# Performance work log

Measured on AMD Instinct MI355X. Metric: run time of the kernel, lower is better.

The kernel has to match this reference:

```python
import jax, jax.numpy as jnp
import numpy as np

N_NODES = 50000
N_EDGES = 800000
NUM_GRAPHS = 4
IN_DIM, HID_DIM, OUT_DIM = 1024, 128, 1
MAX_RISK = 5.0


def gcn_conv(x, W, b, src, dst, n):
    """PyG GCNConv: add self-loops, sym-normalize, gather-GEMM-scatter."""
    loop = jnp.arange(n, dtype=src.dtype)
    s = jnp.concatenate([src, loop])
    d = jnp.concatenate([dst, loop])
    deg = jax.ops.segment_sum(jnp.ones_like(d, dtype=x.dtype), d, num_segments=n)
    dinv = jnp.where(deg > 0, jax.lax.rsqrt(deg), 0.0)
    norm = dinv[s] * dinv[d]  # [E+N]
    xw = x @ W                # dense GEMM first (fewer FLOPs than per-edge)
    msg = xw[s] * norm[:, None]          # irregular gather, [E+N, out]
    out = jax.ops.segment_sum(msg, d, num_segments=n)  # scatter-add
    return out + b


def setup_inputs() -> dict:
    key = jax.random.key(0)
    ks = jax.random.split(key, 12)
    x = jax.random.normal(ks[0], (N_NODES, IN_DIM), dtype=jnp.float32)
    edge_index = jax.random.randint(ks[1], (2, N_EDGES), 0, N_NODES, dtype=jnp.int64)
    batch = jnp.sort(jax.random.randint(ks[2], (N_NODES,), 0, NUM_GRAPHS, dtype=jnp.int64))

    def glorot(k, fan_in, fan_out):
        s = np.sqrt(6.0 / (fan_in + fan_out)).astype(np.float32)
        return jax.random.uniform(k, (fan_in, fan_out), jnp.float32, -s, s)

    params = {
        'W0': glorot(ks[3], IN_DIM, HID_DIM),  'b0': jnp.zeros((HID_DIM,), jnp.float32),
        'W1': glorot(ks[4], HID_DIM, HID_DIM), 'b1': jnp.zeros((HID_DIM,), jnp.float32),
        'W2': glorot(ks[5], HID_DIM, HID_DIM), 'b2': jnp.zeros((HID_DIM,), jnp.float32),
        'Wl1': glorot(ks[6], 2 * HID_DIM, HID_DIM), 'bl1': jnp.zeros((HID_DIM,), jnp.float32),
        'Wl2': glorot(ks[7], HID_DIM, HID_DIM // 2), 'bl2': jnp.zeros((HID_DIM // 2,), jnp.float32),
        'Wl3': glorot(ks[8], HID_DIM // 2, OUT_DIM), 'bl3': jnp.zeros((OUT_DIM,), jnp.float32),
    }
    return dict(x=x, edge_index=edge_index, batch=batch, **params)


def reference(x, edge_index, batch, W0, b0, W1, b1, W2, b2, Wl1, bl1, Wl2, bl2, Wl3, bl3):
    n = x.shape[0]
    src, dst = edge_index[0], edge_index[1]
    h = jax.nn.relu(gcn_conv(x, W0, b0, src, dst, n))
    h = jax.nn.relu(gcn_conv(h, W1, b1, src, dst, n))
    h = jax.nn.relu(gcn_conv(h, W2, b2, src, dst, n))
    # global max pool + global mean pool per graph
    gmax = jax.ops.segment_max(h, batch, num_segments=NUM_GRAPHS)
    gsum = jax.ops.segment_sum(h, batch, num_segments=NUM_GRAPHS)
    cnt = jax.ops.segment_sum(jnp.ones((n,), h.dtype), batch, num_segments=NUM_GRAPHS)
    gmean = gsum / jnp.maximum(cnt, 1.0)[:, None]
    g = jnp.concatenate([gmax, gmean], axis=1)  # [G, 2*hid]
    g = jax.nn.relu(g @ Wl1 + bl1)
    g = jax.nn.relu(g @ Wl2 + bl2)
    out = g @ Wl3 + bl3
    return jnp.minimum(out, MAX_RISK)
```

## Files before the change

kernel.cpp:

```cpp
#include <hip/hip_runtime.h>
#include <math.h>

#define HID 128
#define NGRAPH 4

typedef int idx_t;
typedef float f32x4 __attribute__((ext_vector_type(4)));
typedef _Float16 h8 __attribute__((ext_vector_type(8)));

__global__ __launch_bounds__(256) void k_count(const idx_t* __restrict__ dst,
                                               int* __restrict__ cnt, int E) {
  int e = blockIdx.x * 256 + threadIdx.x;
  if (e < E) atomicAdd(&cnt[dst[e]], 1);
}

#define SC 1024
__global__ __launch_bounds__(256) void k_scan1(const int* __restrict__ cnt,
                                               int* __restrict__ bsum, int n) {
  __shared__ int sh[256];
  int base = blockIdx.x * SC + threadIdx.x * 4;
  int s = 0;
#pragma unroll
  for (int j = 0; j < 4; ++j) { int i = base + j; if (i < n) s += cnt[i]; }
  sh[threadIdx.x] = s;
  __syncthreads();
  for (int o = 128; o > 0; o >>= 1) {
    if (threadIdx.x < o) sh[threadIdx.x] += sh[threadIdx.x + o];
    __syncthreads();
  }
  if (threadIdx.x == 0) bsum[blockIdx.x] = sh[0];
}

__global__ __launch_bounds__(64) void k_scan2(const int* __restrict__ bsum,
                                              int* __restrict__ boff,
                                              int* __restrict__ off, int nb, int n) {
  int lane = threadIdx.x;
  int v = (lane < nb) ? bsum[lane] : 0;
  for (int d = 1; d < 64; d <<= 1) {
    int t = __shfl_up(v, d);
    if (lane >= d) v += t;
  }
  int ex = __shfl_up(v, 1);
  if (lane == 0) ex = 0;
  if (lane < nb) boff[lane] = ex;
  if (lane == nb - 1) off[n] = v;
}

__global__ __launch_bounds__(256) void k_scan3(const int* __restrict__ cnt,
                                               const int* __restrict__ boff,
                                               int* __restrict__ off,
                                               float* __restrict__ dinv, int n) {
  __shared__ int sh[256];
  int base = blockIdx.x * SC + threadIdx.x * 4;
  int c[4];
  int s = 0;
#pragma unroll
  for (int j = 0; j < 4; ++j) {
    int i = base + j;
    c[j] = (i < n) ? cnt[i] : 0;
    s += c[j];
  }
  sh[threadIdx.x] = s;
  __syncthreads();
  for (int o = 1; o < 256; o <<= 1) {
    int t = (threadIdx.x >= (unsigned)o) ? sh[threadIdx.x - o] : 0;
    __syncthreads();
    sh[threadIdx.x] += t;
    __syncthreads();
  }
  int ex = sh[threadIdx.x] - s + boff[blockIdx.x];
#pragma unroll
  for (int j = 0; j < 4; ++j) {
    int i = base + j;
    if (i < n) {
      off[i] = ex;
      dinv[i] = 1.0f / sqrtf((float)c[j] + 1.0f);
      ex += c[j];
    }
  }
}

__global__ __launch_bounds__(256) void k_fill(const idx_t* __restrict__ src,
                                              const idx_t* __restrict__ dst,
                                              const int* __restrict__ off,
                                              const float* __restrict__ dinv,
                                              int* __restrict__ fillc,
                                              int2* __restrict__ edata, int E) {
  int e = blockIdx.x * 256 + threadIdx.x;
  if (e < E) {
    int s = src[e], d = dst[e];
    int p = atomicAdd(&fillc[d], 1);
    float w = dinv[s] * dinv[d];
    edata[off[d] + p] = make_int2(s, __float_as_int(w));
  }
}

__global__ __launch_bounds__(256) void k_wsplitf(const float* __restrict__ W,
                                                 _Float16* __restrict__ Wh,
                                                 _Float16* __restrict__ Wl, int K) {
  int i = blockIdx.x * 256 + threadIdx.x;
  if (i >= K * HID) return;
  int j = i & 7, lane = (i >> 3) & 63, ni = (i >> 9) & 7, t = i >> 12;
  int k = t * 32 + (lane >> 4) * 8 + j;
  int col = ni * 16 + (lane & 15);
  float f = W[(size_t)k * HID + col];
  _Float16 h = (_Float16)f;
  Wh[i] = h;
  Wl[i] = (_Float16)(f - (float)h);
}

template <int K, bool F32>
__global__ __launch_bounds__(256, 4) void k_gemm5(const void* __restrict__ Xv,
                                                  const _Float16* __restrict__ Wfh,
                                                  const _Float16* __restrict__ Wfl,
                                                  _Float16* __restrict__ Y16, int M) {
  constexpr int KPW = K / 4;
  constexpr int NT = KPW / 32;
  const int tid = threadIdx.x;
  const int wid = tid >> 6, lane = tid & 63;
  const int lrow = lane & 15, kg = lane >> 4;
  const int row0 = blockIdx.x * 32;
  const int ra = row0 + lrow, rb = row0 + 16 + lrow;
  const int rca = (ra < M) ? ra : 0, rcb = (rb < M) ? rb : 0;
  const float* xf0 = (const float*)Xv + (size_t)rca * K + wid * KPW + kg * 8;
  const float* xf1 = (const float*)Xv + (size_t)rcb * K + wid * KPW + kg * 8;
  const _Float16* xg0 = (const _Float16*)Xv + (size_t)rca * K + wid * KPW + kg * 8;
  const _Float16* xg1 = (const _Float16*)Xv + (size_t)rcb * K + wid * KPW + kg * 8;

  f32x4 acc[2][8] = {};

#pragma unroll
  for (int t = 0; t < NT; ++t) {
    const int kk = t * 32;
    h8 ah0, al0, ah1, al1;
    if (F32) {
      float4 a0 = *(const float4*)(xf0 + kk);
      float4 a1 = *(const float4*)(xf0 + kk + 4);
      float4 a2 = *(const float4*)(xf1 + kk);
      float4 a3 = *(const float4*)(xf1 + kk + 4);
      float t0[8] = {a0.x, a0.y, a0.z, a0.w, a1.x, a1.y, a1.z, a1.w};
      float t1[8] = {a2.x, a2.y, a2.z, a2.w, a3.x, a3.y, a3.z, a3.w};
#pragma unroll
      for (int j = 0; j < 8; ++j) {
        _Float16 h0 = (_Float16)t0[j], h1 = (_Float16)t1[j];
        ah0[j] = h0; al0[j] = (_Float16)(t0[j] - (float)h0);
        ah1[j] = h1; al1[j] = (_Float16)(t1[j] - (float)h1);
      }
    } else {
      ah0 = *(const h8*)(xg0 + kk);
      ah1 = *(const h8*)(xg1 + kk);
    }
    const size_t fb = (size_t)((wid * NT + t) * 8) * 512 + lane * 8;
#pragma unroll
    for (int ni = 0; ni < 8; ++ni) {
      h8 bh = *(const h8*)(Wfh + fb + ni * 512);
      h8 bl = *(const h8*)(Wfl + fb + ni * 512);
      acc[0][ni] = __builtin_amdgcn_mfma_f32_16x16x32_f16(ah0, bh, acc[0][ni], 0, 0, 0);
      acc[1][ni] = __builtin_amdgcn_mfma_f32_16x16x32_f16(ah1, bh, acc[1][ni], 0, 0, 0);
      if (F32) {
        acc[0][ni] = __builtin_amdgcn_mfma_f32_16x16x32_f16(al0, bh, acc[0][ni], 0, 0, 0);
        acc[1][ni] = __builtin_amdgcn_mfma_f32_16x16x32_f16(al1, bh, acc[1][ni], 0, 0, 0);
      }
      acc[0][ni] = __builtin_amdgcn_mfma_f32_16x16x32_f16(ah0, bl, acc[0][ni], 0, 0, 0);
      acc[1][ni] = __builtin_amdgcn_mfma_f32_16x16x32_f16(ah1, bl, acc[1][ni], 0, 0, 0);
    }
  }

  __shared__ float red[32][132];
  for (int w = 0; w < 4; ++w) {
    if (wid == w) {
#pragma unroll
      for (int mi = 0; mi < 2; ++mi)
#pragma unroll
        for (int ni = 0; ni < 8; ++ni)
#pragma unroll
          for (int rr = 0; rr < 4; ++rr) {
            int r = mi * 16 + kg * 4 + rr, c = ni * 16 + lrow;
            if (w == 0) red[r][c] = acc[mi][ni][rr];
            else red[r][c] += acc[mi][ni][rr];
          }
    }
    __syncthreads();
  }
  int r = tid >> 3, c0 = (tid & 7) * 16;
  int grow = row0 + r;
  if (grow < M) {
    h8 o0, o1;
#pragma unroll
    for (int q = 0; q < 8; ++q) {
      o0[q] = (_Float16)red[r][c0 + q];
      o1[q] = (_Float16)red[r][c0 + 8 + q];
    }
    *(h8*)&Y16[(size_t)grow * HID + c0] = o0;
    *(h8*)&Y16[(size_t)grow * HID + c0 + 8] = o1;
  }
}

__global__ __launch_bounds__(256) void k_agg16(const _Float16* __restrict__ xh,
                                               const float* __restrict__ dinv,
                                               const int* __restrict__ off,
                                               const int2* __restrict__ edata,
                                               const float* __restrict__ bias,
                                               _Float16* __restrict__ hout, int n) {
  int v = blockIdx.x * 4 + (threadIdx.x >> 6);
  if (v >= n) return;
  int lane = threadIdx.x & 63;
  int grp = lane >> 3, gl = lane & 7;
  int fb = gl * 16;
  float acc[16] = {0.f, 0.f, 0.f, 0.f, 0.f, 0.f, 0.f, 0.f,
                   0.f, 0.f, 0.f, 0.f, 0.f, 0.f, 0.f, 0.f};
  int j0 = off[v], j1 = off[v + 1];
  for (int j = j0 + grp; j < j1; j += 8) {
    int2 e = edata[j];
    float w = __int_as_float(e.y);
    h8 m0 = *(const h8*)&xh[(size_t)e.x * HID + fb];
    h8 m1 = *(const h8*)&xh[(size_t)e.x * HID + fb + 8];
#pragma unroll
    for (int q = 0; q < 8; ++q) {
      acc[q] = fmaf(w, (float)m0[q], acc[q]);
      acc[8 + q] = fmaf(w, (float)m1[q], acc[8 + q]);
    }
  }
#pragma unroll
  for (int q = 0; q < 16; ++q) {
    acc[q] += __shfl_xor(acc[q], 8);
    acc[q] += __shfl_xor(acc[q], 16);
    acc[q] += __shfl_xor(acc[q], 32);
  }
  if (grp == 0) {
    float dv = dinv[v], dv2 = dv * dv;
    h8 s0 = *(const h8*)&xh[(size_t)v * HID + fb];
    h8 s1 = *(const h8*)&xh[(size_t)v * HID + fb + 8];
    h8 o0, o1;
#pragma unroll
    for (int q = 0; q < 8; ++q) {
      float a0 = fmaxf(fmaf(dv2, (float)s0[q], acc[q]) + bias[fb + q], 0.f);
      float a1 = fmaxf(fmaf(dv2, (float)s1[q], acc[8 + q]) + bias[fb + 8 + q], 0.f);
      o0[q] = (_Float16)a0;
      o1[q] = (_Float16)a1;
    }
    *(h8*)&hout[(size_t)v * HID + fb] = o0;
    *(h8*)&hout[(size_t)v * HID + fb + 8] = o1;
  }
}

__global__ __launch_bounds__(256) void k_gcnt(const idx_t* __restrict__ batch,
                                              int* __restrict__ gcnt, int n) {
  __shared__ int h[NGRAPH];
  int tid = threadIdx.x;
  if (tid < NGRAPH) h[tid] = 0;
  __syncthreads();
  int i = blockIdx.x * 256 + tid;
  if (i < n) atomicAdd(&h[batch[i]], 1);
  __syncthreads();
  if (tid < NGRAPH && h[tid]) atomicAdd(&gcnt[tid], h[tid]);
}

__global__ __launch_bounds__(128) void k_pool(const _Float16* __restrict__ h,
                                              const idx_t* __restrict__ batch,
                                              float* __restrict__ gmax,
                                              float* __restrict__ gsum, int n) {
  int f = threadIdx.x;
  int v0 = blockIdx.x * 128;
  int cur = -1;
  float mx = 0.f, sm = 0.f;
  for (int i = 0; i < 128; ++i) {
    int v = v0 + i;
    if (v >= n) break;
    int g = batch[v];
    if (g != cur) {
      if (cur >= 0) {
        atomicMax((int*)&gmax[cur * HID + f], __float_as_int(mx));
        atomicAdd(&gsum[cur * HID + f], sm);
      }
      cur = g; mx = 0.f; sm = 0.f;
    }
    float val = (float)h[(size_t)v * HID + f];
    mx = fmaxf(mx, val);
    sm += val;
  }
  if (cur >= 0) {
    atomicMax((int*)&gmax[cur * HID + f], __float_as_int(mx));
    atomicAdd(&gsum[cur * HID + f], sm);
  }
}

__global__ __launch_bounds__(256) void k_mlp(const float* __restrict__ gmax,
                                             const float* __restrict__ gsum,
                                             const int* __restrict__ gcnt,
                                             const float* __restrict__ Wl1,
                                             const float* __restrict__ bl1,
                                             const float* __restrict__ Wl2,
                                             const float* __restrict__ bl2,
                                             const float* __restrict__ Wl3,
                                             const float* __restrict__ bl3,
                                             float* __restrict__ out) {
  __shared__ float G[NGRAPH][2 * HID];
  __shared__ float H1[NGRAPH][HID];
  __shared__ float H2[NGRAPH][HID / 2];
  int t = threadIdx.x;
  for (int i = t; i < NGRAPH * 2 * HID; i += 256) {
    int gi = i >> 8, j = i & 255;
    float val;
    if (j < HID) val = gmax[gi * HID + j];
    else val = gsum[gi * HID + (j - HID)] / fmaxf((float)gcnt[gi], 1.0f);
    G[gi][j] = val;
  }
  __syncthreads();
  for (int i = t; i < NGRAPH * HID; i += 256) {
    int gi = i >> 7, j = i & 127;
    float a = bl1[j];
    for (int k = 0; k < 2 * HID; ++k) a = fmaf(G[gi][k], Wl1[k * HID + j], a);
    H1[gi][j] = fmaxf(a, 0.f);
  }
  __syncthreads();
  {
    int gi = t >> 6, j = t & 63;
    float a = bl2[j];
    for (int k = 0; k < HID; ++k) a = fmaf(H1[gi][k], Wl2[k * 64 + j], a);
    H2[gi][j] = fmaxf(a, 0.f);
  }
  __syncthreads();
  if (t < NGRAPH) {
    float a = bl3[0];
    for (int k = 0; k < 64; ++k) a = fmaf(H2[t][k], Wl3[k], a);
    out[t] = fminf(a, 5.0f);
  }
}

extern "C" void kernel_launch(void* const* d_in, const int* in_sizes, int n_in,
                              void* d_out, int out_size, void* d_ws, size_t ws_size,
                              hipStream_t stream) {
  const float* x   = (const float*)d_in[0];
  const idx_t* ei  = (const idx_t*)d_in[1];
  const idx_t* bat = (const idx_t*)d_in[2];
  const float* W0 = (const float*)d_in[3];  const float* b0 = (const float*)d_in[4];
  const float* W1 = (const float*)d_in[5];  const float* b1 = (const float*)d_in[6];
  const float* W2 = (const float*)d_in[7];  const float* b2 = (const float*)d_in[8];
  const float* Wl1 = (const float*)d_in[9];  const float* bl1 = (const float*)d_in[10];
  const float* Wl2 = (const float*)d_in[11]; const float* bl2 = (const float*)d_in[12];
  const float* Wl3 = (const float*)d_in[13]; const float* bl3 = (const float*)d_in[14];
  float* out = (float*)d_out;

  const int N = in_sizes[2];
  const int E = in_sizes[1] / 2;
  const idx_t* srcv = ei;
  const idx_t* dstv = ei + E;
  const int nb = (N + SC - 1) / SC;

  char* ws = (char*)d_ws;
  size_t o = 0;
  auto alloc = [&](size_t bytes) -> void* {
    void* p = ws + o;
    o = (o + bytes + 255) & ~(size_t)255;
    return p;
  };
  _Float16* xh  = (_Float16*)alloc((size_t)N * HID * 2);
  _Float16* h16 = (_Float16*)alloc((size_t)N * HID * 2);
  float* dinv = (float*)alloc((size_t)N * 4);
  int* cnt    = (int*)alloc((size_t)N * 4);
  int* off    = (int*)alloc((size_t)(N + 1) * 4);
  int* fillc  = (int*)alloc((size_t)N * 4);
  int2* edata = (int2*)alloc((size_t)E * 8);
  int* bsum   = (int*)alloc(64 * 4);
  int* boff   = (int*)alloc(64 * 4);
  _Float16* Wh0 = (_Float16*)alloc((size_t)1024 * HID * 2);
  _Float16* Wl0 = (_Float16*)alloc((size_t)1024 * HID * 2);
  _Float16* Wh1 = (_Float16*)alloc((size_t)HID * HID * 2);
  _Float16* Wlo1 = (_Float16*)alloc((size_t)HID * HID * 2);
  _Float16* Wh2 = (_Float16*)alloc((size_t)HID * HID * 2);
  _Float16* Wlo2 = (_Float16*)alloc((size_t)HID * HID * 2);
  float* gmax = (float*)alloc(NGRAPH * HID * 4);
  float* gsum = (float*)alloc(NGRAPH * HID * 4);
  int* gcnt   = (int*)alloc(NGRAPH * 4);

  hipMemsetAsync(cnt, 0, (size_t)N * 4, stream);
  hipMemsetAsync(fillc, 0, (size_t)N * 4, stream);
  hipMemsetAsync(gmax, 0, NGRAPH * HID * 4, stream);
  hipMemsetAsync(gsum, 0, NGRAPH * HID * 4, stream);
  hipMemsetAsync(gcnt, 0, NGRAPH * 4, stream);

  k_wsplitf<<<(1024 * HID + 255) / 256, 256, 0, stream>>>(W0, Wh0, Wl0, 1024);
  k_wsplitf<<<(HID * HID + 255) / 256, 256, 0, stream>>>(W1, Wh1, Wlo1, HID);
  k_wsplitf<<<(HID * HID + 255) / 256, 256, 0, stream>>>(W2, Wh2, Wlo2, HID);

  k_count<<<(E + 255) / 256, 256, 0, stream>>>(dstv, cnt, E);
  k_scan1<<<nb, 256, 0, stream>>>(cnt, bsum, N);
  k_scan2<<<1, 64, 0, stream>>>(bsum, boff, off, nb, N);
  k_scan3<<<nb, 256, 0, stream>>>(cnt, boff, off, dinv, N);
  k_fill<<<(E + 255) / 256, 256, 0, stream>>>(srcv, dstv, off, dinv, fillc, edata, E);

  const int gblk = (N + 31) / 32;
  const int ablk = (N + 3) / 4;
  k_gemm5<1024, true><<<gblk, 256, 0, stream>>>(x, Wh0, Wl0, xh, N);
  k_agg16<<<ablk, 256, 0, stream>>>(xh, dinv, off, edata, b0, h16, N);
  k_gemm5<HID, false><<<gblk, 256, 0, stream>>>(h16, Wh1, Wlo1, xh, N);
  k_agg16<<<ablk, 256, 0, stream>>>(xh, dinv, off, edata, b1, h16, N);
  k_gemm5<HID, false><<<gblk, 256, 0, stream>>>(h16, Wh2, Wlo2, xh, N);
  k_agg16<<<ablk, 256, 0, stream>>>(xh, dinv, off, edata, b2, h16, N);

  k_gcnt<<<(N + 255) / 256, 256, 0, stream>>>(bat, gcnt, N);
  k_pool<<<(N + 127) / 128, 128, 0, stream>>>(h16, bat, gmax, gsum, N);
  k_mlp<<<1, 256, 0, stream>>>(gmax, gsum, gcnt, Wl1, bl1, Wl2, bl2, Wl3, bl3, out);
}
```

Measured before the change: 371.1 us.

## Stage A tile through swizzled LDS with coalesced loads and 16-row blocks

The GEMM kernel now loads each block's 16-row activation tile with fully coalesced row-wise loads. It splits fp32 inputs into fp16 hi/lo parts once and stores them in XOR-swizzled shared memory, replacing per-wave strided global reads of 32 rows. Blocks shrink from 32 to 16 rows, which halves register accumulators but doubles the number of times the weight fragments are read from global/L2. For K=1024 the LDS footprint grows to about 72KB per block, which limits occupancy, and launch bounds are lowered to 2 blocks per SM.

```diff
diff --git a/kernel.cpp b/kernel.cpp
--- a/kernel.cpp
+++ b/kernel.cpp
@@ -7,6 +7,7 @@
 typedef int idx_t;
 typedef float f32x4 __attribute__((ext_vector_type(4)));
 typedef _Float16 h8 __attribute__((ext_vector_type(8)));
+typedef _Float16 h4 __attribute__((ext_vector_type(4)));
 
 __global__ __launch_bounds__(256) void k_count(const idx_t* __restrict__ dst,
                                                int* __restrict__ cnt, int E) {
@@ -110,89 +111,94 @@
 }
 
 template <int K, bool F32>
-__global__ __launch_bounds__(256, 4) void k_gemm5(const void* __restrict__ Xv,
+__global__ __launch_bounds__(256, 2) void k_gemm6(const void* __restrict__ Xv,
                                                   const _Float16* __restrict__ Wfh,
                                                   const _Float16* __restrict__ Wfl,
                                                   _Float16* __restrict__ Y16, int M) {
   constexpr int KPW = K / 4;
   constexpr int NT = KPW / 32;
+  __shared__ _Float16 AhL[16 * K];
+  __shared__ _Float16 AlL[F32 ? 16 * K : 16];
+  __shared__ float red[16][132];
   const int tid = threadIdx.x;
   const int wid = tid >> 6, lane = tid & 63;
   const int lrow = lane & 15, kg = lane >> 4;
-  const int row0 = blockIdx.x * 32;
-  const int ra = row0 + lrow, rb = row0 + 16 + lrow;
-  const int rca = (ra < M) ? ra : 0, rcb = (rb < M) ? rb : 0;
-  const float* xf0 = (const float*)Xv + (size_t)rca * K + wid * KPW + kg * 8;
-  const float* xf1 = (const float*)Xv + (size_t)rcb * K + wid * KPW + kg * 8;
-  const _Float16* xg0 = (const _Float16*)Xv + (size_t)rca * K + wid * KPW + kg * 8;
-  const _Float16* xg1 = (const _Float16*)Xv + (size_t)rcb * K + wid * KPW + kg * 8;
-
-  f32x4 acc[2][8] = {};
-
+  const int row0 = blockIdx.x * 16;
+
+  if (F32) {
+    const float* X = (const float*)Xv;
+#pragma unroll
+    for (int r = 0; r < 16; ++r) {
+      int grow = row0 + r;
+      int grc = (grow < M) ? grow : (M - 1);
+      float4 v = *(const float4*)&X[(size_t)grc * K + tid * 4];
+      h4 hv, lv;
+      float tf[4] = {v.x, v.y, v.z, v.w};
+#pragma unroll
+      for (int j = 0; j < 4; ++j) {
+        _Float16 hh = (_Float16)tf[j];
+        hv[j] = hh;
+        lv[j] = (_Float16)(tf[j] - (float)hh);
+      }
+      int swb = (tid * 8) ^ ((r & 7) << 4);
+      *(h4*)((char*)AhL + r * (2 * K) + swb) = hv;
+      *(h4*)((char*)AlL + r * (2 * K) + swb) = lv;
+    }
+  } else {
+    const _Float16* X = (const _Float16*)Xv;
+    int r = (tid * 16) / (2 * K);
+    int kb = (tid * 16) % (2 * K);
+    int grow = row0 + r;
+    int grc = (grow < M) ? grow : (M - 1);
+    h8 v = *(const h8*)&X[(size_t)grc * K + kb / 2];
+    int swb = kb ^ ((r & 7) << 4);
+    *(h8*)((char*)AhL + r * (2 * K) + swb) = v;
+  }
+  __syncthreads();
+
+  f32x4 acc[8] = {};
 #pragma unroll
   for (int t = 0; t < NT; ++t) {
-    const int kk = t * 32;
-    h8 ah0, al0, ah1, al1;
-    if (F32) {
-      float4 a0 = *(const float4*)(xf0 + kk);
-      float4 a1 = *(const float4*)(xf0 + kk + 4);
-      float4 a2 = *(const float4*)(xf1 + kk);
-      float4 a3 = *(const float4*)(xf1 + kk + 4);
-      float t0[8] = {a0.x, a0.y, a0.z, a0.w, a1.x, a1.y, a1.z, a1.w};
-      float t1[8] = {a2.x, a2.y, a2.z, a2.w, a3.x, a3.y, a3.z, a3.w};
-#pragma unroll
-      for (int j = 0; j < 8; ++j) {
-        _Float16 h0 = (_Float16)t0[j], h1 = (_Float16)t1[j];
-        ah0[j] = h0; al0[j] = (_Float16)(t0[j] - (float)h0);
-        ah1[j] = h1; al1[j] = (_Float16)(t1[j] - (float)h1);
-      }
-    } else {
-      ah0 = *(const h8*)(xg0 + kk);
-      ah1 = *(const h8*)(xg1 + kk);
+    const int kk = wid * KPW + t * 32;
+    h8 ah, al;
+    {
+      int kb = (kk + kg * 8) * 2;
+      int swb = kb ^ ((lrow & 7) << 4);
+      ah = *(const h8*)((const char*)AhL + lrow * (2 * K) + swb);
+      if (F32) al = *(const h8*)((const char*)AlL + lrow * (2 * K) + swb);
     }
     const size_t fb = (size_t)((wid * NT + t) * 8) * 512 + lane * 8;
 #pragma unroll
     for (int ni = 0; ni < 8; ++ni) {
       h8 bh = *(const h8*)(Wfh + fb + ni * 512);
       h8 bl = *(const h8*)(Wfl + fb + ni * 512);
-      acc[0][ni] = __builtin_amdgcn_mfma_f32_16x16x32_f16(ah0, bh, acc[0][ni], 0, 0, 0);
-      acc[1][ni] = __builtin_amdgcn_mfma_f32_16x16x32_f16(ah1, bh, acc[1][ni], 0, 0, 0);
-      if (F32) {
-        acc[0][ni] = __builtin_amdgcn_mfma_f32_16x16x32_f16(al0, bh, acc[0][ni], 0, 0, 0);
-        acc[1][ni] = __builtin_amdgcn_mfma_f32_16x16x32_f16(al1, bh, acc[1][ni], 0, 0, 0);
-      }
-      acc[0][ni] = __builtin_amdgcn_mfma_f32_16x16x32_f16(ah0, bl, acc[0][ni], 0, 0, 0);
-      acc[1][ni] = __builtin_amdgcn_mfma_f32_16x16x32_f16(ah1, bl, acc[1][ni], 0, 0, 0);
-    }
-  }
-
-  __shared__ float red[32][132];
+      acc[ni] = __builtin_amdgcn_mfma_f32_16x16x32_f16(ah, bh, acc[ni], 0, 0, 0);
+      if (F32)
+        acc[ni] = __builtin_amdgcn_mfma_f32_16x16x32_f16(al, bh, acc[ni], 0, 0, 0);
+      acc[ni] = __builtin_amdgcn_mfma_f32_16x16x32_f16(ah, bl, acc[ni], 0, 0, 0);
+    }
+  }
+
   for (int w = 0; w < 4; ++w) {
     if (wid == w) {
 #pragma unroll
-      for (int mi = 0; mi < 2; ++mi)
-#pragma unroll
-        for (int ni = 0; ni < 8; ++ni)
-#pragma unroll
-          for (int rr = 0; rr < 4; ++rr) {
-            int r = mi * 16 + kg * 4 + rr, c = ni * 16 + lrow;
-            if (w == 0) red[r][c] = acc[mi][ni][rr];
-            else red[r][c] += acc[mi][ni][rr];
-          }
+      for (int ni = 0; ni < 8; ++ni)
+#pragma unroll
+        for (int rr = 0; rr < 4; ++rr) {
+          int r = kg * 4 + rr, c = ni * 16 + lrow;
+          if (w == 0) red[r][c] = acc[ni][rr];
+          else red[r][c] += acc[ni][rr];
+        }
     }
     __syncthreads();
   }
-  int r = tid >> 3, c0 = (tid & 7) * 16;
+  int r = tid >> 4, c0 = (tid & 15) * 8;
   int grow = row0 + r;
   if (grow < M) {
-    h8 o0, o1;
-#pragma unroll
-    for (int q = 0; q < 8; ++q) {
-      o0[q] = (_Float16)red[r][c0 + q];
-      o1[q] = (_Float16)red[r][c0 + 8 + q];
-    }
-    *(h8*)&Y16[(size_t)grow * HID + c0] = o0;
-    *(h8*)&Y16[(size_t)grow * HID + c0 + 8] = o1;
+    h8 o;
+#pragma unroll
+    for (int q = 0; q < 8; ++q) o[q] = (_Float16)red[r][c0 + q];
+    *(h8*)&Y16[(size_t)grow * HID + c0] = o;
   }
 }
 
@@ -390,13 +396,13 @@
   k_scan3<<<nb, 256, 0, stream>>>(cnt, boff, off, dinv, N);
   k_fill<<<(E + 255) / 256, 256, 0, stream>>>(srcv, dstv, off, dinv, fillc, edata, E);
 
-  const int gblk = (N + 31) / 32;
+  const int gblk = (N + 15) / 16;
   const int ablk = (N + 3) / 4;
-  k_gemm5<1024, true><<<gblk, 256, 0, stream>>>(x, Wh0, Wl0, xh, N);
+  k_gemm6<1024, true><<<gblk, 256, 0, stream>>>(x, Wh0, Wl0, xh, N);
   k_agg16<<<ablk, 256, 0, stream>>>(xh, dinv, off, edata, b0, h16, N);
-  k_gemm5<HID, false><<<gblk, 256, 0, stream>>>(h16, Wh1, Wlo1, xh, N);
+  k_gemm6<HID, false><<<gblk, 256, 0, stream>>>(h16, Wh1, Wlo1, xh, N);
   k_agg16<<<ablk, 256, 0, stream>>>(xh, dinv, off, edata, b1, h16, N);
-  k_gemm5<HID, false><<<gblk, 256, 0, stream>>>(h16, Wh2, Wlo2, xh, N);
+  k_gemm6<HID, false><<<gblk, 256, 0, stream>>>(h16, Wh2, Wlo2, xh, N);
   k_agg16<<<ablk, 256, 0, stream>>>(xh, dinv, off, edata, b2, h16, N);
 
   k_gcnt<<<(N + 255) / 256, 256, 0, stream>>>(bat, gcnt, N);
```

Result: slower. 447.5 us (+20.6%).
